# Performance work log

Measured on AMD Instinct MI355X. Metric: run time of the kernel, lower is better.

Reference implementation:

```python
import jax, jax.numpy as jnp
import numpy as np

N = 100000   # nodes
E = 1600000  # edges (avg degree 16)
F_IN = 128
H = 128
C = 16


def setup_inputs() -> dict:
    key = jax.random.key(0)
    ks = jax.random.split(key, 13)
    s = 1.0 / np.sqrt(H)
    return {
        "x": jax.random.normal(ks[0], (N, F_IN), jnp.float32),
        "edge_index": jax.random.randint(ks[1], (2, E), 0, N, jnp.int32),
        "edge_weight": jax.random.uniform(ks[2], (E,), jnp.float32),
        "W1": jax.random.normal(ks[3], (F_IN, H), jnp.float32) * s,
        "b1": jnp.zeros((H,), jnp.float32),
        "W2": jax.random.normal(ks[4], (H, H), jnp.float32) * s,
        "b2": jnp.zeros((H,), jnp.float32),
        "Wg": jax.random.normal(ks[5], (H, H), jnp.float32) * s,
        "att_src": jax.random.normal(ks[6], (H,), jnp.float32) * s,
        "att_dst": jax.random.normal(ks[7], (H,), jnp.float32) * s,
        "bg": jnp.zeros((H,), jnp.float32),
        "Wc": jax.random.normal(ks[8], (H, C), jnp.float32) * s,
        "bc": jnp.zeros((C,), jnp.float32),
    }


def reference(x, edge_index, edge_weight, W1, b1, W2, b2, Wg, att_src, att_dst, bg, Wc, bc):
    n = x.shape[0]
    loop = jnp.arange(n, dtype=edge_index.dtype)
    src = jnp.concatenate([edge_index[0], loop])   # self loops (PyG default)
    dst = jnp.concatenate([edge_index[1], loop])
    ew = jnp.concatenate([edge_weight, jnp.ones((n,), x.dtype)])  # loop weight 1

    # GCN normalization: D^{-1/2} A D^{-1/2}, degree on dst with edge weights
    deg = jax.ops.segment_sum(ew, dst, num_segments=n)
    dinv = jnp.where(deg > 0, jax.lax.rsqrt(deg), 0.0)
    norm = dinv[src] * ew * dinv[dst]              # [E+N]

    def gcn(h, W, b):
        h = h @ W                                   # [N,H]
        agg = jax.ops.segment_sum(h[src] * norm[:, None], dst, num_segments=n)
        return agg + b

    h = jax.nn.relu(gcn(x, W1, b1))
    h = jax.nn.relu(gcn(h, W2, b2))                 # dropout inert in eval

    # GATConv, heads=1
    g = h @ Wg                                      # [N,H]
    a = jax.nn.leaky_relu((g @ att_src)[src] + (g @ att_dst)[dst], 0.2)
    amax = jax.ops.segment_max(a, dst, num_segments=n)
    ex = jnp.exp(a - amax[dst])
    denom = jax.ops.segment_sum(ex, dst, num_segments=n)
    alpha = ex / denom[dst]                         # edge softmax per dst
    out = jax.ops.segment_sum(g[src] * alpha[:, None], dst, num_segments=n) + bg
    out = jax.nn.relu(out)
    return out @ Wc + bc
```

## Files before the change

### kernel.cpp

```cpp
#include <hip/hip_runtime.h>
#include <hip/hip_fp16.h>

#define FIN 128
#define HD 128
#define COUT 16

#define SLOT_CAP 48
#define CS_BLOCKS 512
#define CB_SHIFT 9
#define CB_SIZE 512
#define CAP_B 10240
#define GMK_CELLS 64

typedef _Float16 half8 __attribute__((ext_vector_type(8)));
typedef float floatx4 __attribute__((ext_vector_type(4)));

__device__ __forceinline__ float lrelu02(float x) { return x > 0.f ? x : 0.2f * x; }

union U4H8 { uint4 q; __half2 h2[4]; };
union UQH8 { uint4 q; half8 h; _Float16 e[8]; };

__device__ __forceinline__ void h8f(const uint4 q, float* f) {
    U4H8 u; u.q = q;
    float2 a0 = __half22float2(u.h2[0]);
    float2 a1 = __half22float2(u.h2[1]);
    float2 a2 = __half22float2(u.h2[2]);
    float2 a3 = __half22float2(u.h2[3]);
    f[0] = a0.x; f[1] = a0.y; f[2] = a1.x; f[3] = a1.y;
    f[4] = a2.x; f[5] = a2.y; f[6] = a3.x; f[7] = a3.y;
}

__device__ __forceinline__ unsigned fkey(float f) {
    unsigned u = __float_as_uint(f);
    return (u & 0x80000000u) ? ~u : (u | 0x80000000u);
}
__device__ __forceinline__ float funkey(unsigned k) {
    return (k & 0x80000000u) ? __uint_as_float(k ^ 0x80000000u)
                             : __uint_as_float(~k);
}

__global__ void k_setup(const float* __restrict__ W1, const float* __restrict__ W2,
                        const float* __restrict__ Wg, __half* __restrict__ w1z,
                        __half* __restrict__ w2z, __half* __restrict__ wgz,
                        int* __restrict__ cur, unsigned* __restrict__ gmk) {
    int b = blockIdx.x;
    if (b < 24) {
        const float* W = (b < 8) ? W1 : (b < 16) ? W2 : Wg;
        __half* outp   = (b < 8) ? w1z : (b < 16) ? w2z : wgz;
        int t = (b & 7) * 256 + threadIdx.x;
        int lane = t & 63;
        int kc = (t >> 6) & 3;
        int nt = t >> 8;
        int kbase = kc * 32 + (lane >> 4) * 8;
        int col = nt * 16 + (lane & 15);
        UQH8 u;
#pragma unroll
        for (int j = 0; j < 8; j++)
            u.e[j] = (_Float16)W[(kbase + j) * 128 + col];
        ((uint4*)outp)[t] = u.q;
    } else {
        cur[threadIdx.x] = 0;
        for (int i = threadIdx.x; i < GMK_CELLS * 16; i += 256)
            gmk[i] = 0u;
    }
}

__global__ __launch_bounds__(256)
void k_cscatter(const int* __restrict__ src, const int* __restrict__ dst,
                const float* __restrict__ ew, int* __restrict__ cur,
                int2* __restrict__ coarseBuf, int e) {
    __shared__ int lcnt[256], lbase[256], lpos[256];
    int tid = threadIdx.x;
    lcnt[tid] = 0; lpos[tid] = 0;
    __syncthreads();
    int chunk = (e + CS_BLOCKS - 1) / CS_BLOCKS;
    int s0 = blockIdx.x * chunk;
    int s1 = min(s0 + chunk, e);
    for (int i = s0 + tid; i < s1; i += 256)
        atomicAdd(&lcnt[dst[i] >> CB_SHIFT], 1);
    __syncthreads();
    if (lcnt[tid] > 0) lbase[tid] = atomicAdd(&cur[tid], lcnt[tid]);
    __syncthreads();
    for (int i = s0 + tid; i < s1; i += 256) {
        int d = dst[i];
        int b = d >> CB_SHIFT;
        int pos = lbase[b] + atomicAdd(&lpos[b], 1);
        if (pos < CAP_B)
            coarseBuf[(size_t)b * CAP_B + pos] =
                make_int2(((d & (CB_SIZE - 1)) << 17) | src[i], __float_as_int(ew[i]));
    }
}

__device__ __forceinline__
void gemm_body_f32(int blk, const float* __restrict__ A, const __half* __restrict__ Wz,
                   __half* __restrict__ Out, int n) {
    int wave = threadIdx.x >> 6;
    int lane = threadIdx.x & 63;
    int m0 = blk * 64 + wave * 16;
    if (m0 >= n) return;
    int m = lane & 15;
    int quad = lane >> 4;

    half8 a[4];
#pragma unroll
    for (int kc = 0; kc < 4; kc++) {
        const float* p = &A[(size_t)(m0 + m) * 128 + kc * 32 + quad * 8];
        float4 f0 = *(const float4*)p;
        float4 f1 = *(const float4*)(p + 4);
        UQH8 u;
        u.e[0] = (_Float16)f0.x; u.e[1] = (_Float16)f0.y;
        u.e[2] = (_Float16)f0.z; u.e[3] = (_Float16)f0.w;
        u.e[4] = (_Float16)f1.x; u.e[5] = (_Float16)f1.y;
        u.e[6] = (_Float16)f1.z; u.e[7] = (_Float16)f1.w;
        a[kc] = u.h;
    }

    floatx4 acc[8];
#pragma unroll
    for (int nt = 0; nt < 8; nt++) acc[nt] = (floatx4){0.f, 0.f, 0.f, 0.f};

    const uint4* Wv = (const uint4*)Wz;
#pragma unroll
    for (int kc = 0; kc < 4; kc++) {
#pragma unroll
        for (int nt = 0; nt < 8; nt++) {
            UQH8 u;
            u.q = Wv[(nt * 4 + kc) * 64 + lane];
            acc[nt] = __builtin_amdgcn_mfma_f32_16x16x32_f16(a[kc], u.h, acc[nt], 0, 0, 0);
        }
    }
#pragma unroll
    for (int nt = 0; nt < 8; nt++) {
#pragma unroll
        for (int reg = 0; reg < 4; reg++) {
            Out[(size_t)(m0 + quad * 4 + reg) * 128 + nt * 16 + m] =
                __float2half(acc[nt][reg]);
        }
    }
}

__launch_bounds__(256)
__global__ void k_fine_gemm(const int2* __restrict__ coarseBuf, const int* __restrict__ cur,
                            int NB, int2* __restrict__ slots, int* __restrict__ cnt,
                            float* __restrict__ dinv, int n,
                            const float* __restrict__ x, const __half* __restrict__ w1z,
                            __half* __restrict__ buf0) {
    __shared__ int lcnt[CB_SIZE];
    __shared__ float lsum[CB_SIZE];
    if ((int)blockIdx.x < NB) {
        int b = blockIdx.x;
        int tid = threadIdx.x;
        for (int i = tid; i < CB_SIZE; i += 256) { lcnt[i] = 0; lsum[i] = 0.f; }
        __syncthreads();
        int ecnt = min(cur[b], CAP_B);
        size_t e0 = (size_t)b * CAP_B;
        for (int e = tid; e < ecnt; e += 256) {
            int2 it = coarseBuf[e0 + e];
            int dl = (it.x >> 17) & (CB_SIZE - 1);
            int src = it.x & 0x1FFFF;
            int pos = atomicAdd(&lcnt[dl], 1);
            atomicAdd(&lsum[dl], __int_as_float(it.y));
            if (pos < SLOT_CAP) {
                int node = (b << CB_SHIFT) + dl;
                slots[(size_t)node * SLOT_CAP + pos] = make_int2(src, it.y);
            }
        }
        __syncthreads();
        int nodeBase = b << CB_SHIFT;
        for (int i = tid; i < CB_SIZE; i += 256) {
            int node = nodeBase + i;
            if (node < n) {
                cnt[node] = min(lcnt[i], SLOT_CAP);
                dinv[node] = rsqrtf(1.0f + lsum[i]);
            }
        }
    } else {
        gemm_body_f32(blockIdx.x - NB, x, w1z, buf0, n);
    }
}

__device__ __forceinline__
void gather_body(int node, int lane, const int* __restrict__ cnt,
                 const int2* __restrict__ slots, const uint4* __restrict__ tv,
                 const float* __restrict__ dinv, const float* __restrict__ b,
                 float* __restrict__ fout) {
    float dd = dinv[node];
    float sw = dd * dd;
    float acc[8];
    {
        uint4 q = tv[(size_t)node * 16 + lane];
        float f[8]; h8f(q, f);
#pragma unroll
        for (int j = 0; j < 8; j++) acc[j] = f[j] * sw;
    }
    int r0 = (int)((size_t)node * SLOT_CAP);
    int r1 = r0 + cnt[node];
    int e = r0;
    for (; e + 8 <= r1; e += 8) {
        int2 c[8];
        float dv[8];
        uint4 v[8];
#pragma unroll
        for (int j = 0; j < 8; j++) c[j] = slots[e + j];
#pragma unroll
        for (int j = 0; j < 8; j++) dv[j] = dinv[c[j].x];
#pragma unroll
        for (int j = 0; j < 8; j++) v[j] = tv[(size_t)c[j].x * 16 + lane];
#pragma unroll
        for (int j = 0; j < 8; j++) {
            float w = dv[j] * __int_as_float(c[j].y) * dd;
            float f[8]; h8f(v[j], f);
#pragma unroll
            for (int k = 0; k < 8; k++) acc[k] = fmaf(f[k], w, acc[k]);
        }
    }
    for (; e + 2 <= r1; e += 2) {
        int2 c0 = slots[e], c1 = slots[e + 1];
        float dv0 = dinv[c0.x], dv1 = dinv[c1.x];
        uint4 v0 = tv[(size_t)c0.x * 16 + lane];
        uint4 v1 = tv[(size_t)c1.x * 16 + lane];
        float w0 = dv0 * __int_as_float(c0.y) * dd;
        float w1 = dv1 * __int_as_float(c1.y) * dd;
        float f0[8], f1[8]; h8f(v0, f0); h8f(v1, f1);
#pragma unroll
        for (int k = 0; k < 8; k++) acc[k] = fmaf(f0[k], w0, acc[k]);
#pragma unroll
        for (int k = 0; k < 8; k++) acc[k] = fmaf(f1[k], w1, acc[k]);
    }
    if (e < r1) {
        int2 c = slots[e];
        uint4 v = tv[(size_t)c.x * 16 + lane];
        float w = dinv[c.x] * __int_as_float(c.y) * dd;
        float f[8]; h8f(v, f);
#pragma unroll
        for (int k = 0; k < 8; k++) acc[k] = fmaf(f[k], w, acc[k]);
    }
    const float4* b4 = (const float4*)b;
    float4 bb0 = b4[lane * 2], bb1 = b4[lane * 2 + 1];
    fout[0] = fmaxf(acc[0] + bb0.x, 0.f);
    fout[1] = fmaxf(acc[1] + bb0.y, 0.f);
    fout[2] = fmaxf(acc[2] + bb0.z, 0.f);
    fout[3] = fmaxf(acc[3] + bb0.w, 0.f);
    fout[4] = fmaxf(acc[4] + bb1.x, 0.f);
    fout[5] = fmaxf(acc[5] + bb1.y, 0.f);
    fout[6] = fmaxf(acc[6] + bb1.z, 0.f);
    fout[7] = fmaxf(acc[7] + bb1.w, 0.f);
}

template <bool ATTN>
__launch_bounds__(256)
__global__ void k_gather_gemm(const int* __restrict__ cnt, const int2* __restrict__ slots,
                              const __half* __restrict__ t, const float* __restrict__ dinv,
                              const float* __restrict__ b, const __half* __restrict__ Wz,
                              __half* __restrict__ Out,
                              const float* __restrict__ attS, const float* __restrict__ attD,
                              float* __restrict__ as_, float* __restrict__ ad_,
                              unsigned* __restrict__ gmaxKey, int n) {
    __shared__ __half stage[16][136];
    __shared__ float redS[4][16], redD[4][16];
    int tid = threadIdx.x;
    int nl = tid >> 4;
    int lane16 = tid & 15;
    int node = blockIdx.x * 16 + nl;

    if (node < n) {
        float f[8];
        gather_body(node, lane16, cnt, slots, (const uint4*)t, dinv, b, f);
        UQH8 u;
#pragma unroll
        for (int j = 0; j < 8; j++) u.e[j] = (_Float16)f[j];
        *(uint4*)&stage[nl][lane16 * 8] = u.q;
    } else {
        UQH8 u;
#pragma unroll
        for (int j = 0; j < 8; j++) u.e[j] = (_Float16)0.f;
        *(uint4*)&stage[nl][lane16 * 8] = u.q;
    }
    __syncthreads();

    int wave = tid >> 6;
    int lane = tid & 63;
    int m = lane & 15;
    int quad = lane >> 4;
    int m0 = blockIdx.x * 16;

    half8 a[4];
#pragma unroll
    for (int kc = 0; kc < 4; kc++)
        a[kc] = *(const half8*)&stage[m][kc * 32 + quad * 8];

    floatx4 acc[2];
    acc[0] = (floatx4){0.f, 0.f, 0.f, 0.f};
    acc[1] = (floatx4){0.f, 0.f, 0.f, 0.f};
    const uint4* Wv = (const uint4*)Wz;
#pragma unroll
    for (int t2 = 0; t2 < 2; t2++) {
        int nt = wave * 2 + t2;
#pragma unroll
        for (int kc = 0; kc < 4; kc++) {
            UQH8 u;
            u.q = Wv[(nt * 4 + kc) * 64 + lane];
            acc[t2] = __builtin_amdgcn_mfma_f32_16x16x32_f16(a[kc], u.h, acc[t2], 0, 0, 0);
        }
    }
#pragma unroll
    for (int t2 = 0; t2 < 2; t2++) {
        int col = (wave * 2 + t2) * 16 + m;
#pragma unroll
        for (int reg = 0; reg < 4; reg++) {
            int row = m0 + quad * 4 + reg;
            if (row < n)
                Out[(size_t)row * 128 + col] = __float2half(acc[t2][reg]);
        }
    }

    if (ATTN) {
        float sv0 = attS[(wave * 2 + 0) * 16 + m], sv1 = attS[(wave * 2 + 1) * 16 + m];
        float dv0 = attD[(wave * 2 + 0) * 16 + m], dv1 = attD[(wave * 2 + 1) * 16 + m];
#pragma unroll
        for (int reg = 0; reg < 4; reg++) {
            float s = acc[0][reg] * sv0 + acc[1][reg] * sv1;
            float d = acc[0][reg] * dv0 + acc[1][reg] * dv1;
#pragma unroll
            for (int k = 8; k >= 1; k >>= 1) {
                s += __shfl_xor(s, k, 64);
                d += __shfl_xor(d, k, 64);
            }
            if (m == 0) {
                redS[wave][quad * 4 + reg] = s;
                redD[wave][quad * 4 + reg] = d;
            }
        }
        __syncthreads();
        if (tid < 16) {
            int nd = m0 + tid;
            unsigned key = 0u;
            if (nd < n) {
                float sv = redS[0][tid] + redS[1][tid] + redS[2][tid] + redS[3][tid];
                float dv = redD[0][tid] + redD[1][tid] + redD[2][tid] + redD[3][tid];
                as_[nd] = sv;
                ad_[nd] = dv;
                key = fkey(sv);
            }
#pragma unroll
            for (int k = 8; k >= 1; k >>= 1) {
                unsigned o = (unsigned)__shfl_xor((int)key, k, 64);
                key = key > o ? key : o;
            }
            if (tid == 0)
                atomicMax(&gmaxKey[(blockIdx.x & (GMK_CELLS - 1)) << 4], key);
        }
    }
}

__launch_bounds__(256)
__global__ void k_gat_final(const int* __restrict__ cnt, const int2* __restrict__ slots,
                            const __half* __restrict__ g, const float* __restrict__ as_,
                            const float* __restrict__ ad_,
                            const unsigned* __restrict__ gmaxKey,
                            const float* __restrict__ bg,
                            const float* __restrict__ Wc, const float* __restrict__ bc,
                            float* __restrict__ out, int n) {
    __shared__ float Wcs[128 * 16];
    __shared__ float bcs[16];
    __shared__ float stage[16][136];
    __shared__ float gmaxS;
    int tid = threadIdx.x;
    for (int i = tid; i < 128 * 16; i += 256) Wcs[i] = Wc[i];
    if (tid < 16) bcs[tid] = bc[tid];

    if (tid < 64) {
        unsigned k = gmaxKey[tid << 4];
#pragma unroll
        for (int d = 32; d >= 1; d >>= 1) {
            unsigned o = (unsigned)__shfl_xor((int)k, d, 64);
            k = k > o ? k : o;
        }
        if (tid == 0) gmaxS = funkey(k);
    }
    __syncthreads();
    float gmax = gmaxS;

    int idx = blockIdx.x * 256 + tid;
    int node = idx >> 4;
    int lane = idx & 15;
    int nl = tid >> 4;

    if (node < n) {
        int r0 = (int)((size_t)node * SLOT_CAP);
        int r1 = r0 + cnt[node];
        float ad_d = ad_[node];
        float c = lrelu02(gmax + ad_d);
        const uint4* gv = (const uint4*)g;
        float ex = __expf(lrelu02(as_[node] + ad_d) - c);
        float den = ex;
        float acc[8];
        {
            uint4 q = gv[(size_t)node * 16 + lane];
            float f[8]; h8f(q, f);
#pragma unroll
            for (int j = 0; j < 8; j++) acc[j] = ex * f[j];
        }
        int e = r0;
        for (; e + 8 <= r1; e += 8) {
            int s[8];
            uint4 u[8];
#pragma unroll
            for (int j = 0; j < 8; j++) s[j] = slots[e + j].x;
#pragma unroll
            for (int j = 0; j < 8; j++) u[j] = gv[(size_t)s[j] * 16 + lane];
#pragma unroll
            for (int j = 0; j < 8; j++) {
                float w = __expf(lrelu02(as_[s[j]] + ad_d) - c);
                den += w;
                float f[8]; h8f(u[j], f);
#pragma unroll
                for (int k = 0; k < 8; k++) acc[k] = fmaf(f[k], w, acc[k]);
            }
        }
        for (; e + 2 <= r1; e += 2) {
            int s0 = slots[e].x, s1 = slots[e + 1].x;
            uint4 u0 = gv[(size_t)s0 * 16 + lane];
            uint4 u1 = gv[(size_t)s1 * 16 + lane];
            float w0 = __expf(lrelu02(as_[s0] + ad_d) - c);
            float w1 = __expf(lrelu02(as_[s1] + ad_d) - c);
            den += w0 + w1;
            float f0[8], f1[8]; h8f(u0, f0); h8f(u1, f1);
#pragma unroll
            for (int k = 0; k < 8; k++) acc[k] = fmaf(f0[k], w0, acc[k]);
#pragma unroll
            for (int k = 0; k < 8; k++) acc[k] = fmaf(f1[k], w1, acc[k]);
        }
        if (e < r1) {
            int s = slots[e].x;
            uint4 u = gv[(size_t)s * 16 + lane];
            float w = __expf(lrelu02(as_[s] + ad_d) - c);
            den += w;
            float f[8]; h8f(u, f);
#pragma unroll
            for (int k = 0; k < 8; k++) acc[k] = fmaf(f[k], w, acc[k]);
        }
        float inv = 1.0f / den;
        const float4* bg4 = (const float4*)bg;
        float4 b0 = bg4[lane * 2], b1 = bg4[lane * 2 + 1];
        float* sp = &stage[nl][lane * 8];
        sp[0] = fmaxf(acc[0] * inv + b0.x, 0.f);
        sp[1] = fmaxf(acc[1] * inv + b0.y, 0.f);
        sp[2] = fmaxf(acc[2] * inv + b0.z, 0.f);
        sp[3] = fmaxf(acc[3] * inv + b0.w, 0.f);
        sp[4] = fmaxf(acc[4] * inv + b1.x, 0.f);
        sp[5] = fmaxf(acc[5] * inv + b1.y, 0.f);
        sp[6] = fmaxf(acc[6] * inv + b1.z, 0.f);
        sp[7] = fmaxf(acc[7] * inv + b1.w, 0.f);
    }
    __syncthreads();
    int nl2 = tid >> 4;
    int col = tid & 15;
    int onode = blockIdx.x * 16 + nl2;
    if (onode >= n) return;
    float accp = bcs[col];
    const float* sp = stage[nl2];
#pragma unroll 8
    for (int k = 0; k < 128; k++)
        accp = fmaf(sp[k], Wcs[k * 16 + col], accp);
    out[(size_t)onode * 16 + col] = accp;
}

extern "C" void kernel_launch(void* const* d_in, const int* in_sizes, int n_in,
                              void* d_out, int out_size, void* d_ws, size_t ws_size,
                              hipStream_t stream) {
    const float* x      = (const float*)d_in[0];
    const int*   eidx   = (const int*)d_in[1];
    const float* ew     = (const float*)d_in[2];
    const float* W1     = (const float*)d_in[3];
    const float* b1     = (const float*)d_in[4];
    const float* W2     = (const float*)d_in[5];
    const float* b2     = (const float*)d_in[6];
    const float* Wg     = (const float*)d_in[7];
    const float* attS   = (const float*)d_in[8];
    const float* attD   = (const float*)d_in[9];
    const float* bg     = (const float*)d_in[10];
    const float* Wc     = (const float*)d_in[11];
    const float* bc     = (const float*)d_in[12];

    const int N = in_sizes[0] / FIN;
    const int E = in_sizes[2];
    const int* src = eidx;
    const int* dst = eidx + E;
    const int NB = (N + CB_SIZE - 1) >> CB_SHIFT;

    char* base = (char*)d_ws;
    size_t off = 0;
    auto carve = [&](size_t bytes) {
        char* q = base + off;
        off = (off + bytes + 255) & ~(size_t)255;
        return (void*)q;
    };
    int*    cnt       = (int*)carve((size_t)N * 4);
    int*    cur       = (int*)carve(256 * 4);
    unsigned* gmk     = (unsigned*)carve((size_t)GMK_CELLS * 16 * 4);
    int2*   coarseBuf = (int2*)carve((size_t)NB * CAP_B * 8);
    int2*   slots     = (int2*)carve((size_t)N * SLOT_CAP * 8);
    float*  dinv      = (float*)carve((size_t)N * 4);
    float*  as_       = (float*)carve((size_t)N * 4);
    float*  ad_       = (float*)carve((size_t)N * 4);
    __half* w1z       = (__half*)carve((size_t)128 * 128 * 2);
    __half* w2z       = (__half*)carve((size_t)128 * 128 * 2);
    __half* wgz       = (__half*)carve((size_t)128 * 128 * 2);
    __half* buf0      = (__half*)carve((size_t)N * 128 * 2);
    __half* buf1      = (__half*)carve((size_t)N * 128 * 2);

    const int B = 256;
    dim3 blk(B);
    int fusedGrid = (N + 15) / 16;
    int gemmGrid = (N + 63) / 64;

    k_setup<<<25, blk, 0, stream>>>(W1, W2, Wg, w1z, w2z, wgz, cur, gmk);
    k_cscatter<<<CS_BLOCKS, blk, 0, stream>>>(src, dst, ew, cur, coarseBuf, E);
    k_fine_gemm<<<NB + gemmGrid, blk, 0, stream>>>(coarseBuf, cur, NB, slots, cnt,
                                                   dinv, N, x, w1z, buf0);

    k_gather_gemm<false><<<fusedGrid, blk, 0, stream>>>(cnt, slots, buf0, dinv, b1, w2z,
                                                        buf1, nullptr, nullptr,
                                                        nullptr, nullptr, nullptr, N);
    k_gather_gemm<true><<<fusedGrid, blk, 0, stream>>>(cnt, slots, buf1, dinv, b2, wgz,
                                                       buf0, attS, attD, as_, ad_, gmk, N);
    k_gat_final<<<fusedGrid, blk, 0, stream>>>(cnt, slots, buf0, as_, ad_, gmk, bg,
                                               Wc, bc, (float*)d_out, N);
}
```

Baseline: 427.8 us.

## Fold GCN source-side normalization into GEMM epilogues to drop per-edge dinv gathers

Computes node degrees with global atomics during the coarse scatter so the first GEMM can pre-scale its output rows by dinv, and the second fused GEMM now scales its rows by dinv as well. The gather loops then use only the raw edge weight, with the destination dinv applied once at the end. This removes a random dinv[src] load and two multiplies per edge. It adds a memset and 1.6M global float atomics in the scatter kernel. The GAT loop also hoists the attention-source loads ahead of the feature loads for better memory-level parallelism.

```diff
diff --git a/kernel.cpp b/kernel.cpp
--- a/kernel.cpp
+++ b/kernel.cpp
@@ -68,7 +68,7 @@
 __global__ __launch_bounds__(256)
 void k_cscatter(const int* __restrict__ src, const int* __restrict__ dst,
                 const float* __restrict__ ew, int* __restrict__ cur,
-                int2* __restrict__ coarseBuf, int e) {
+                int2* __restrict__ coarseBuf, float* __restrict__ deg, int e) {
     __shared__ int lcnt[256], lbase[256], lpos[256];
     int tid = threadIdx.x;
     lcnt[tid] = 0; lpos[tid] = 0;
@@ -83,17 +83,19 @@
     __syncthreads();
     for (int i = s0 + tid; i < s1; i += 256) {
         int d = dst[i];
+        float w = ew[i];
+        atomicAdd(&deg[d], w);
         int b = d >> CB_SHIFT;
         int pos = lbase[b] + atomicAdd(&lpos[b], 1);
         if (pos < CAP_B)
             coarseBuf[(size_t)b * CAP_B + pos] =
-                make_int2(((d & (CB_SIZE - 1)) << 17) | src[i], __float_as_int(ew[i]));
+                make_int2(((d & (CB_SIZE - 1)) << 17) | src[i], __float_as_int(w));
     }
 }
 
 __device__ __forceinline__
 void gemm_body_f32(int blk, const float* __restrict__ A, const __half* __restrict__ Wz,
-                   __half* __restrict__ Out, int n) {
+                   __half* __restrict__ Out, const float* __restrict__ deg, int n) {
     int wave = threadIdx.x >> 6;
     int lane = threadIdx.x & 63;
     int m0 = blk * 64 + wave * 16;
@@ -130,11 +132,13 @@
         }
     }
 #pragma unroll
-    for (int nt = 0; nt < 8; nt++) {
-#pragma unroll
-        for (int reg = 0; reg < 4; reg++) {
-            Out[(size_t)(m0 + quad * 4 + reg) * 128 + nt * 16 + m] =
-                __float2half(acc[nt][reg]);
+    for (int reg = 0; reg < 4; reg++) {
+        int row = m0 + quad * 4 + reg;
+        if (row < n) {
+            float dsc = rsqrtf(1.0f + deg[row]);
+#pragma unroll
+            for (int nt = 0; nt < 8; nt++)
+                Out[(size_t)row * 128 + nt * 16 + m] = __float2half(acc[nt][reg] * dsc);
         }
     }
 }
@@ -142,15 +146,14 @@
 __launch_bounds__(256)
 __global__ void k_fine_gemm(const int2* __restrict__ coarseBuf, const int* __restrict__ cur,
                             int NB, int2* __restrict__ slots, int* __restrict__ cnt,
-                            float* __restrict__ dinv, int n,
+                            float* __restrict__ dinv, const float* __restrict__ deg, int n,
                             const float* __restrict__ x, const __half* __restrict__ w1z,
                             __half* __restrict__ buf0) {
     __shared__ int lcnt[CB_SIZE];
-    __shared__ float lsum[CB_SIZE];
     if ((int)blockIdx.x < NB) {
         int b = blockIdx.x;
         int tid = threadIdx.x;
-        for (int i = tid; i < CB_SIZE; i += 256) { lcnt[i] = 0; lsum[i] = 0.f; }
+        for (int i = tid; i < CB_SIZE; i += 256) lcnt[i] = 0;
         __syncthreads();
         int ecnt = min(cur[b], CAP_B);
         size_t e0 = (size_t)b * CAP_B;
@@ -159,7 +162,6 @@
             int dl = (it.x >> 17) & (CB_SIZE - 1);
             int src = it.x & 0x1FFFF;
             int pos = atomicAdd(&lcnt[dl], 1);
-            atomicAdd(&lsum[dl], __int_as_float(it.y));
             if (pos < SLOT_CAP) {
                 int node = (b << CB_SHIFT) + dl;
                 slots[(size_t)node * SLOT_CAP + pos] = make_int2(src, it.y);
@@ -171,11 +173,11 @@
             int node = nodeBase + i;
             if (node < n) {
                 cnt[node] = min(lcnt[i], SLOT_CAP);
-                dinv[node] = rsqrtf(1.0f + lsum[i]);
+                dinv[node] = rsqrtf(1.0f + deg[node]);
             }
         }
     } else {
-        gemm_body_f32(blockIdx.x - NB, x, w1z, buf0, n);
+        gemm_body_f32(blockIdx.x - NB, x, w1z, buf0, deg, n);
     }
 }
 
@@ -185,30 +187,24 @@
                  const float* __restrict__ dinv, const float* __restrict__ b,
                  float* __restrict__ fout) {
     float dd = dinv[node];
-    float sw = dd * dd;
     float acc[8];
     {
         uint4 q = tv[(size_t)node * 16 + lane];
-        float f[8]; h8f(q, f);
-#pragma unroll
-        for (int j = 0; j < 8; j++) acc[j] = f[j] * sw;
+        h8f(q, acc);
     }
     int r0 = (int)((size_t)node * SLOT_CAP);
     int r1 = r0 + cnt[node];
     int e = r0;
     for (; e + 8 <= r1; e += 8) {
         int2 c[8];
-        float dv[8];
         uint4 v[8];
 #pragma unroll
         for (int j = 0; j < 8; j++) c[j] = slots[e + j];
 #pragma unroll
-        for (int j = 0; j < 8; j++) dv[j] = dinv[c[j].x];
-#pragma unroll
         for (int j = 0; j < 8; j++) v[j] = tv[(size_t)c[j].x * 16 + lane];
 #pragma unroll
         for (int j = 0; j < 8; j++) {
-            float w = dv[j] * __int_as_float(c[j].y) * dd;
+            float w = __int_as_float(c[j].y);
             float f[8]; h8f(v[j], f);
 #pragma unroll
             for (int k = 0; k < 8; k++) acc[k] = fmaf(f[k], w, acc[k]);
@@ -216,11 +212,10 @@
     }
     for (; e + 2 <= r1; e += 2) {
         int2 c0 = slots[e], c1 = slots[e + 1];
-        float dv0 = dinv[c0.x], dv1 = dinv[c1.x];
         uint4 v0 = tv[(size_t)c0.x * 16 + lane];
         uint4 v1 = tv[(size_t)c1.x * 16 + lane];
-        float w0 = dv0 * __int_as_float(c0.y) * dd;
-        float w1 = dv1 * __int_as_float(c1.y) * dd;
+        float w0 = __int_as_float(c0.y);
+        float w1 = __int_as_float(c1.y);
         float f0[8], f1[8]; h8f(v0, f0); h8f(v1, f1);
 #pragma unroll
         for (int k = 0; k < 8; k++) acc[k] = fmaf(f0[k], w0, acc[k]);
@@ -230,21 +225,21 @@
     if (e < r1) {
         int2 c = slots[e];
         uint4 v = tv[(size_t)c.x * 16 + lane];
-        float w = dinv[c.x] * __int_as_float(c.y) * dd;
+        float w = __int_as_float(c.y);
         float f[8]; h8f(v, f);
 #pragma unroll
         for (int k = 0; k < 8; k++) acc[k] = fmaf(f[k], w, acc[k]);
     }
     const float4* b4 = (const float4*)b;
     float4 bb0 = b4[lane * 2], bb1 = b4[lane * 2 + 1];
-    fout[0] = fmaxf(acc[0] + bb0.x, 0.f);
-    fout[1] = fmaxf(acc[1] + bb0.y, 0.f);
-    fout[2] = fmaxf(acc[2] + bb0.z, 0.f);
-    fout[3] = fmaxf(acc[3] + bb0.w, 0.f);
-    fout[4] = fmaxf(acc[4] + bb1.x, 0.f);
-    fout[5] = fmaxf(acc[5] + bb1.y, 0.f);
-    fout[6] = fmaxf(acc[6] + bb1.z, 0.f);
-    fout[7] = fmaxf(acc[7] + bb1.w, 0.f);
+    fout[0] = fmaxf(fmaf(dd, acc[0], bb0.x), 0.f);
+    fout[1] = fmaxf(fmaf(dd, acc[1], bb0.y), 0.f);
+    fout[2] = fmaxf(fmaf(dd, acc[2], bb0.z), 0.f);
+    fout[3] = fmaxf(fmaf(dd, acc[3], bb0.w), 0.f);
+    fout[4] = fmaxf(fmaf(dd, acc[4], bb1.x), 0.f);
+    fout[5] = fmaxf(fmaf(dd, acc[5], bb1.y), 0.f);
+    fout[6] = fmaxf(fmaf(dd, acc[6], bb1.z), 0.f);
+    fout[7] = fmaxf(fmaf(dd, acc[7], bb1.w), 0.f);
 }
 
 template <bool ATTN>
@@ -304,13 +299,15 @@
         }
     }
 #pragma unroll
-    for (int t2 = 0; t2 < 2; t2++) {
-        int col = (wave * 2 + t2) * 16 + m;
-#pragma unroll
-        for (int reg = 0; reg < 4; reg++) {
-            int row = m0 + quad * 4 + reg;
-            if (row < n)
-                Out[(size_t)row * 128 + col] = __float2half(acc[t2][reg]);
+    for (int reg = 0; reg < 4; reg++) {
+        int row = m0 + quad * 4 + reg;
+        if (row < n) {
+            float dsc = ATTN ? 1.0f : dinv[row];
+#pragma unroll
+            for (int t2 = 0; t2 < 2; t2++) {
+                int col = (wave * 2 + t2) * 16 + m;
+                Out[(size_t)row * 128 + col] = __float2half(acc[t2][reg] * dsc);
+            }
         }
     }
 
@@ -404,14 +401,17 @@
         int e = r0;
         for (; e + 8 <= r1; e += 8) {
             int s[8];
+            float av[8];
             uint4 u[8];
 #pragma unroll
             for (int j = 0; j < 8; j++) s[j] = slots[e + j].x;
 #pragma unroll
+            for (int j = 0; j < 8; j++) av[j] = as_[s[j]];
+#pragma unroll
             for (int j = 0; j < 8; j++) u[j] = gv[(size_t)s[j] * 16 + lane];
 #pragma unroll
             for (int j = 0; j < 8; j++) {
-                float w = __expf(lrelu02(as_[s[j]] + ad_d) - c);
+                float w = __expf(lrelu02(av[j] + ad_d) - c);
                 den += w;
                 float f[8]; h8f(u[j], f);
 #pragma unroll
@@ -502,6 +502,7 @@
     int2*   coarseBuf = (int2*)carve((size_t)NB * CAP_B * 8);
     int2*   slots     = (int2*)carve((size_t)N * SLOT_CAP * 8);
     float*  dinv      = (float*)carve((size_t)N * 4);
+    float*  deg       = (float*)carve((size_t)N * 4);
     float*  as_       = (float*)carve((size_t)N * 4);
     float*  ad_       = (float*)carve((size_t)N * 4);
     __half* w1z       = (__half*)carve((size_t)128 * 128 * 2);
@@ -515,10 +516,11 @@
     int fusedGrid = (N + 15) / 16;
     int gemmGrid = (N + 63) / 64;
 
+    hipMemsetAsync(deg, 0, (size_t)N * 4, stream);
     k_setup<<<25, blk, 0, stream>>>(W1, W2, Wg, w1z, w2z, wgz, cur, gmk);
-    k_cscatter<<<CS_BLOCKS, blk, 0, stream>>>(src, dst, ew, cur, coarseBuf, E);
+    k_cscatter<<<CS_BLOCKS, blk, 0, stream>>>(src, dst, ew, cur, coarseBuf, deg, E);
     k_fine_gemm<<<NB + gemmGrid, blk, 0, stream>>>(coarseBuf, cur, NB, slots, cnt,
-                                                   dinv, N, x, w1z, buf0);
+                                                   dinv, deg, N, x, w1z, buf0);
 
     k_gather_gemm<false><<<fusedGrid, blk, 0, stream>>>(cnt, slots, buf0, dinv, b1, w2z,
                                                         buf1, nullptr, nullptr,
```

Measured after the change: 499.2 us. 1.17x slower.

## Replace two-pass coarse bucket scatter with direct global-atomic slot scatter

Applied to the files above, without the earlier changes.

Drops the two-level binning (coarse bucket buffer, then a per-bucket LDS fine scatter) and has each edge atomically claim a slot in its destination node's row in global memory, accumulating degree with a global float atomic. Counters are zeroed with memsets, and a small kernel clamps counts and computes dinv, fused with the first GEMM. This removes the intermediate coarse buffer's write and read traffic but relies on heavy contended global atomics and random scattered slot writes. It also adds a row bound check to the GEMM store and hoists the attention-source loads in the GAT loop ahead of use.

```diff
diff --git a/kernel.cpp b/kernel.cpp
--- a/kernel.cpp
+++ b/kernel.cpp
@@ -6,10 +6,7 @@
 #define COUT 16
 
 #define SLOT_CAP 48
-#define CS_BLOCKS 512
-#define CB_SHIFT 9
-#define CB_SIZE 512
-#define CAP_B 10240
+#define SC_BLOCKS 2048
 #define GMK_CELLS 64
 
 typedef _Float16 half8 __attribute__((ext_vector_type(8)));
@@ -42,7 +39,7 @@
 __global__ void k_setup(const float* __restrict__ W1, const float* __restrict__ W2,
                         const float* __restrict__ Wg, __half* __restrict__ w1z,
                         __half* __restrict__ w2z, __half* __restrict__ wgz,
-                        int* __restrict__ cur, unsigned* __restrict__ gmk) {
+                        unsigned* __restrict__ gmk) {
     int b = blockIdx.x;
     if (b < 24) {
         const float* W = (b < 8) ? W1 : (b < 16) ? W2 : Wg;
@@ -59,35 +56,24 @@
             u.e[j] = (_Float16)W[(kbase + j) * 128 + col];
         ((uint4*)outp)[t] = u.q;
     } else {
-        cur[threadIdx.x] = 0;
         for (int i = threadIdx.x; i < GMK_CELLS * 16; i += 256)
             gmk[i] = 0u;
     }
 }
 
 __global__ __launch_bounds__(256)
-void k_cscatter(const int* __restrict__ src, const int* __restrict__ dst,
-                const float* __restrict__ ew, int* __restrict__ cur,
-                int2* __restrict__ coarseBuf, int e) {
-    __shared__ int lcnt[256], lbase[256], lpos[256];
-    int tid = threadIdx.x;
-    lcnt[tid] = 0; lpos[tid] = 0;
-    __syncthreads();
-    int chunk = (e + CS_BLOCKS - 1) / CS_BLOCKS;
-    int s0 = blockIdx.x * chunk;
-    int s1 = min(s0 + chunk, e);
-    for (int i = s0 + tid; i < s1; i += 256)
-        atomicAdd(&lcnt[dst[i] >> CB_SHIFT], 1);
-    __syncthreads();
-    if (lcnt[tid] > 0) lbase[tid] = atomicAdd(&cur[tid], lcnt[tid]);
-    __syncthreads();
-    for (int i = s0 + tid; i < s1; i += 256) {
+void k_scatter(const int* __restrict__ src, const int* __restrict__ dst,
+               const float* __restrict__ ew, int* __restrict__ cnt,
+               float* __restrict__ deg, int2* __restrict__ slots, int e) {
+    int stride = gridDim.x * 256;
+    for (int i = blockIdx.x * 256 + threadIdx.x; i < e; i += stride) {
         int d = dst[i];
-        int b = d >> CB_SHIFT;
-        int pos = lbase[b] + atomicAdd(&lpos[b], 1);
-        if (pos < CAP_B)
-            coarseBuf[(size_t)b * CAP_B + pos] =
-                make_int2(((d & (CB_SIZE - 1)) << 17) | src[i], __float_as_int(ew[i]));
+        int s = src[i];
+        float w = ew[i];
+        int pos = atomicAdd(&cnt[d], 1);
+        atomicAdd(&deg[d], w);
+        if (pos < SLOT_CAP)
+            slots[(size_t)d * SLOT_CAP + pos] = make_int2(s, __float_as_int(w));
     }
 }
 
@@ -130,52 +116,33 @@
         }
     }
 #pragma unroll
-    for (int nt = 0; nt < 8; nt++) {
-#pragma unroll
-        for (int reg = 0; reg < 4; reg++) {
-            Out[(size_t)(m0 + quad * 4 + reg) * 128 + nt * 16 + m] =
-                __float2half(acc[nt][reg]);
+    for (int reg = 0; reg < 4; reg++) {
+        int row = m0 + quad * 4 + reg;
+        if (row < n) {
+#pragma unroll
+            for (int nt = 0; nt < 8; nt++)
+                Out[(size_t)row * 128 + nt * 16 + m] = __float2half(acc[nt][reg]);
         }
     }
 }
 
 __launch_bounds__(256)
-__global__ void k_fine_gemm(const int2* __restrict__ coarseBuf, const int* __restrict__ cur,
-                            int NB, int2* __restrict__ slots, int* __restrict__ cnt,
-                            float* __restrict__ dinv, int n,
+__global__ void k_dinv_gemm(int* __restrict__ cnt, const float* __restrict__ deg,
+                            float* __restrict__ dinv, int NDB, int n,
                             const float* __restrict__ x, const __half* __restrict__ w1z,
                             __half* __restrict__ buf0) {
-    __shared__ int lcnt[CB_SIZE];
-    __shared__ float lsum[CB_SIZE];
-    if ((int)blockIdx.x < NB) {
-        int b = blockIdx.x;
-        int tid = threadIdx.x;
-        for (int i = tid; i < CB_SIZE; i += 256) { lcnt[i] = 0; lsum[i] = 0.f; }
-        __syncthreads();
-        int ecnt = min(cur[b], CAP_B);
-        size_t e0 = (size_t)b * CAP_B;
-        for (int e = tid; e < ecnt; e += 256) {
-            int2 it = coarseBuf[e0 + e];
-            int dl = (it.x >> 17) & (CB_SIZE - 1);
-            int src = it.x & 0x1FFFF;
-            int pos = atomicAdd(&lcnt[dl], 1);
-            atomicAdd(&lsum[dl], __int_as_float(it.y));
-            if (pos < SLOT_CAP) {
-                int node = (b << CB_SHIFT) + dl;
-                slots[(size_t)node * SLOT_CAP + pos] = make_int2(src, it.y);
+    if ((int)blockIdx.x < NDB) {
+        int node = blockIdx.x * 512 + threadIdx.x;
+#pragma unroll
+        for (int h = 0; h < 2; h++, node += 256) {
+            if (node < n) {
+                int c = cnt[node];
+                if (c > SLOT_CAP) cnt[node] = SLOT_CAP;
+                dinv[node] = rsqrtf(1.0f + deg[node]);
             }
         }
-        __syncthreads();
-        int nodeBase = b << CB_SHIFT;
-        for (int i = tid; i < CB_SIZE; i += 256) {
-            int node = nodeBase + i;
-            if (node < n) {
-                cnt[node] = min(lcnt[i], SLOT_CAP);
-                dinv[node] = rsqrtf(1.0f + lsum[i]);
-            }
-        }
     } else {
-        gemm_body_f32(blockIdx.x - NB, x, w1z, buf0, n);
+        gemm_body_f32(blockIdx.x - NDB, x, w1z, buf0, n);
     }
 }
 
@@ -404,14 +371,17 @@
         int e = r0;
         for (; e + 8 <= r1; e += 8) {
             int s[8];
+            float av[8];
             uint4 u[8];
 #pragma unroll
             for (int j = 0; j < 8; j++) s[j] = slots[e + j].x;
 #pragma unroll
+            for (int j = 0; j < 8; j++) av[j] = as_[s[j]];
+#pragma unroll
             for (int j = 0; j < 8; j++) u[j] = gv[(size_t)s[j] * 16 + lane];
 #pragma unroll
             for (int j = 0; j < 8; j++) {
-                float w = __expf(lrelu02(as_[s[j]] + ad_d) - c);
+                float w = __expf(lrelu02(av[j] + ad_d) - c);
                 den += w;
                 float f[8]; h8f(u[j], f);
 #pragma unroll
@@ -487,7 +457,6 @@
     const int E = in_sizes[2];
     const int* src = eidx;
     const int* dst = eidx + E;
-    const int NB = (N + CB_SIZE - 1) >> CB_SHIFT;
 
     char* base = (char*)d_ws;
     size_t off = 0;
@@ -497,9 +466,8 @@
         return (void*)q;
     };
     int*    cnt       = (int*)carve((size_t)N * 4);
-    int*    cur       = (int*)carve(256 * 4);
+    float*  deg       = (float*)carve((size_t)N * 4);
     unsigned* gmk     = (unsigned*)carve((size_t)GMK_CELLS * 16 * 4);
-    int2*   coarseBuf = (int2*)carve((size_t)NB * CAP_B * 8);
     int2*   slots     = (int2*)carve((size_t)N * SLOT_CAP * 8);
     float*  dinv      = (float*)carve((size_t)N * 4);
     float*  as_       = (float*)carve((size_t)N * 4);
@@ -514,11 +482,13 @@
     dim3 blk(B);
     int fusedGrid = (N + 15) / 16;
     int gemmGrid = (N + 63) / 64;
-
-    k_setup<<<25, blk, 0, stream>>>(W1, W2, Wg, w1z, w2z, wgz, cur, gmk);
-    k_cscatter<<<CS_BLOCKS, blk, 0, stream>>>(src, dst, ew, cur, coarseBuf, E);
-    k_fine_gemm<<<NB + gemmGrid, blk, 0, stream>>>(coarseBuf, cur, NB, slots, cnt,
-                                                   dinv, N, x, w1z, buf0);
+    int NDB = (N + 511) / 512;
+
+    hipMemsetAsync(cnt, 0, (size_t)N * 4, stream);
+    hipMemsetAsync(deg, 0, (size_t)N * 4, stream);
+    k_setup<<<25, blk, 0, stream>>>(W1, W2, Wg, w1z, w2z, wgz, gmk);
+    k_scatter<<<SC_BLOCKS, blk, 0, stream>>>(src, dst, ew, cnt, deg, slots, E);
+    k_dinv_gemm<<<NDB + gemmGrid, blk, 0, stream>>>(cnt, deg, dinv, NDB, N, x, w1z, buf0);
 
     k_gather_gemm<false><<<fusedGrid, blk, 0, stream>>>(cnt, slots, buf0, dinv, b1, w2z,
                                                         buf1, nullptr, nullptr,
```

Result: slower. 547.1 us (+27.9%).
